# Performance work log

Measured on AMD Instinct MI355X. Metric: run time of the kernel, lower is better.

The kernel has to match this reference:

```python
import jax, jax.numpy as jnp
import numpy as np

B, T, E = 2, 4096, 1024
H = 16
D = E // H  # head_len = 64


def setup_inputs() -> dict:
    key = jax.random.key(0)
    ks = jax.random.split(key, 6)
    s = 1.0 / np.sqrt(E)
    return {
        "x": jax.random.normal(ks[0], (B, T, E), dtype=jnp.float32),
        # torch nn.Linear weights: shape (out, in), y = x @ W.T
        "Wq": jax.random.uniform(ks[1], (E, E), jnp.float32, -s, s),
        "Wk": jax.random.uniform(ks[2], (E, E), jnp.float32, -s, s),
        "Wv": jax.random.uniform(ks[3], (E, E), jnp.float32, -s, s),
        "Wo": jax.random.uniform(ks[4], (E, E), jnp.float32, -s, s),
        "bo": jax.random.uniform(ks[5], (E,), jnp.float32, -s, s),
    }


def reference(x, Wq, Wk, Wv, Wo, bo):
    Bx, Tx, Ex = x.shape
    q = x @ Wq.T
    k = x @ Wk.T
    v = x @ Wv.T
    # (B, T, H, D) -> (B, H, T, D)
    q = q.reshape(Bx, Tx, H, D).transpose(0, 2, 1, 3)
    k = k.reshape(Bx, Tx, H, D).transpose(0, 2, 1, 3)
    v = v.reshape(Bx, Tx, H, D).transpose(0, 2, 1, 3)
    # scores: (B, H, T, T), scaled by sqrt(head_len)
    sim = jnp.einsum("bhqd,bhkd->bhqk", q, k) / jnp.sqrt(jnp.float32(D))
    causal = jnp.tril(jnp.ones((Tx, Tx), dtype=bool))  # True = keep
    sim = jnp.where(causal[None, None], sim, -jnp.inf)
    attn = jax.nn.softmax(sim, axis=-1)
    # dropout_rate = 0.0 (eval) -> identity
    out = jnp.einsum("bhqk,bhkd->bhqd", attn, v)
    out = out.transpose(0, 2, 1, 3).reshape(Bx, Tx, Ex)
    return out @ Wo.T + bo
```

## Files before the change

### kernel.cpp

```cpp
#include <hip/hip_runtime.h>

typedef unsigned short bf16_t;
typedef __bf16 bf16x8 __attribute__((ext_vector_type(8)));
typedef float  v4f   __attribute__((ext_vector_type(4)));
typedef float  v16f  __attribute__((ext_vector_type(16)));
typedef unsigned u32x2 __attribute__((ext_vector_type(2)));

__device__ __forceinline__ bf16_t f2bf(float f) {
    union { float f; unsigned u; } a; a.f = f;
    unsigned r = a.u + 0x7FFFu + ((a.u >> 16) & 1u);
    return (bf16_t)(r >> 16);
}

__device__ __forceinline__ unsigned cvtpk(float lo, float hi) {
    unsigned r;
    asm("v_cvt_pk_bf16_f32 %0, %1, %2" : "=v"(r) : "v"(lo), "v"(hi));
    return r;
}

__device__ __forceinline__ v16f zero16() {
    v16f z;
#pragma unroll
    for (int i = 0; i < 16; ++i) z[i] = 0.f;
    return z;
}

#define GL16(g, l) __builtin_amdgcn_global_load_lds( \
    (__attribute__((address_space(1))) void*)(g),    \
    (__attribute__((address_space(3))) void*)(l), 16, 0, 0)

#define QSCALE 0.18033688011f

__global__ __launch_bounds__(256) void cvt_all(
    const float4* __restrict__ x,  const float4* __restrict__ wq,
    const float4* __restrict__ wk, const float4* __restrict__ wv,
    const float4* __restrict__ wo,
    ushort4* __restrict__ xb, ushort4* __restrict__ wqkv, ushort4* __restrict__ wob) {
    int i = blockIdx.x * 256 + threadIdx.x;
    const float4* s; ushort4* d; int off;
    if (i < 2097152) { s = x; d = xb; off = i; }
    else {
        int wdx = (i - 2097152) >> 18;
        off = (i - 2097152) & 262143;
        if      (wdx == 0) { s = wq; d = wqkv; }
        else if (wdx == 1) { s = wk; d = wqkv + 262144; }
        else if (wdx == 2) { s = wv; d = wqkv + 524288; }
        else               { s = wo; d = wob; }
    }
    float4 v = s[off];
    ushort4 o;
    o.x = f2bf(v.x); o.y = f2bf(v.y); o.z = f2bf(v.z); o.w = f2bf(v.w);
    d[off] = o;
}

__global__ __launch_bounds__(512, 4) void gemm_qkv_kernel(
    const bf16_t* __restrict__ A, const bf16_t* __restrict__ W,
    bf16_t* __restrict__ Qb, bf16_t* __restrict__ Kb, bf16_t* __restrict__ Vtb) {
    __shared__ bf16_t SMEM[16384];
    bf16_t* As = SMEM;
    bf16_t* Bs = SMEM + 8192;
    const int tid = threadIdx.x;
    const int w = tid >> 6, lane = tid & 63;
    const int lrow = lane & 15, lq = lane >> 4;
    const int id_ = blockIdx.y * 24 + blockIdx.x;
    const int xcd_ = id_ & 7, r_ = id_ >> 3;
    const int bys = xcd_ * 4 + (r_ & 3), bxs = r_ >> 2;
    const int m0 = bys * 256, n0 = bxs * 128;
    const int srw = lane >> 2;
    const int sk = (lane & 3) * 8;
    const int wm = (w & 3) * 64, wn = (w >> 2) * 64;
    v4f acc[4][4];
#pragma unroll
    for (int i = 0; i < 4; ++i)
#pragma unroll
        for (int j = 0; j < 4; ++j) acc[i][j] = (v4f){0.f, 0.f, 0.f, 0.f};

    for (int k0 = 0; k0 < 1024; k0 += 32) {
        __syncthreads();
#pragma unroll
        for (int c = 0; c < 3; ++c) {
            int u = w * 3 + c;
            if (u < 16)
                GL16(A + (size_t)(m0 + u * 16 + srw) * 1024 + k0 + sk, (char*)As + u * 1024);
            else
                GL16(W + (size_t)(n0 + (u - 16) * 16 + srw) * 1024 + k0 + sk,
                     (char*)Bs + (u - 16) * 1024);
        }
        __syncthreads();
        bf16x8 af[4], bf[4];
#pragma unroll
        for (int i = 0; i < 4; ++i)
            af[i] = *(const bf16x8*)&As[(wm + i * 16 + lrow) * 32 + lq * 8];
#pragma unroll
        for (int j = 0; j < 4; ++j)
            bf[j] = *(const bf16x8*)&Bs[(wn + j * 16 + lrow) * 32 + lq * 8];
#pragma unroll
        for (int i = 0; i < 4; ++i)
#pragma unroll
            for (int j = 0; j < 4; ++j)
                acc[i][j] = __builtin_amdgcn_mfma_f32_16x16x32_bf16(af[i], bf[j],
                                                                    acc[i][j], 0, 0, 0);
    }

    const int x = bxs;
    const int b = m0 >> 12, t0 = m0 & 4095;
    if (x < 8) {
#pragma unroll
        for (int i = 0; i < 4; ++i)
#pragma unroll
            for (int j = 0; j < 4; ++j)
#pragma unroll
                for (int r = 0; r < 4; ++r) {
                    int t = t0 + wm + i * 16 + lq * 4 + r;
                    int n = n0 + wn + j * 16 + lrow;
                    int h = n >> 6, d = n & 63;
                    Qb[(((size_t)b * 16 + h) * 4096 + t) * 64 + d] =
                        f2bf(acc[i][j][r] * QSCALE);
                }
    } else if (x < 16) {
#pragma unroll
        for (int i = 0; i < 4; ++i)
#pragma unroll
            for (int j = 0; j < 4; ++j)
#pragma unroll
                for (int r = 0; r < 4; ++r) {
                    int t = t0 + wm + i * 16 + lq * 4 + r;
                    int nn = n0 + wn + j * 16 + lrow - 1024;
                    int h = nn >> 6, d = nn & 63;
                    Kb[(((size_t)b * 16 + h) * 4096 + t) * 64 + d] = f2bf(acc[i][j][r]);
                }
    } else {
        const int d0 = n0 - 2048;
#pragma unroll 1
        for (int p = 0; p < 2; ++p) {
            __syncthreads();
            if ((w >> 2) == p) {
#pragma unroll
                for (int i = 0; i < 4; ++i)
#pragma unroll
                    for (int j = 0; j < 4; ++j) {
                        int row = j * 16 + lrow;
                        int swz = (row & 7) << 1;
                        int g = (wm >> 2) + i * 4 + lq;
                        uint2 u;
                        u.x = (unsigned)f2bf(acc[i][j][0]) | ((unsigned)f2bf(acc[i][j][1]) << 16);
                        u.y = (unsigned)f2bf(acc[i][j][2]) | ((unsigned)f2bf(acc[i][j][3]) << 16);
                        *(uint2*)&SMEM[row * 256 + ((g ^ swz) << 2)] = u;
                    }
            }
            __syncthreads();
#pragma unroll
            for (int uu = 0; uu < 4; ++uu) {
                int unit = tid + 512 * uu;
                int row = unit >> 5, seg = unit & 31;
                uint4 val = *(const uint4*)&SMEM[row * 256 + ((seg ^ (row & 7)) << 3)];
                *(uint4*)&Vtb[((size_t)b * 1024 + d0 + p * 64 + row) * 4096 + t0 + seg * 8] = val;
            }
        }
    }
}

#define GEMM_MAINLOOP(A_, W_)                                                          \
    __shared__ bf16_t SMEM[8192];                                                      \
    bf16_t* As = SMEM; bf16_t* Bs = SMEM + 4096;                                       \
    const int tid = threadIdx.x;                                                       \
    const int w = tid >> 6, lane = tid & 63;                                           \
    const int lrow = lane & 15, lq = lane >> 4;                                        \
    const int nwg_ = gridDim.x * gridDim.y;                                            \
    const int id_ = blockIdx.y * gridDim.x + blockIdx.x;                               \
    const int sid_ = (id_ & 7) * (nwg_ >> 3) + (id_ >> 3);                             \
    const int bxs = sid_ % gridDim.x, bys = sid_ / gridDim.x;                          \
    const int m0 = bys * 128, n0 = bxs * 128;                                          \
    const int srow = w * 16 + (lane >> 2);                                             \
    const int sk = (lane & 3) * 8;                                                     \
    const int wm = (w & 1) * 64, wn = (w >> 1) * 64;                                   \
    v4f acc[4][4];                                                                     \
    _Pragma("unroll") for (int i = 0; i < 4; ++i)                                      \
        _Pragma("unroll") for (int j = 0; j < 4; ++j)                                  \
            acc[i][j] = (v4f){0.f, 0.f, 0.f, 0.f};                                     \
    for (int k0 = 0; k0 < 1024; k0 += 32) {                                            \
        __syncthreads();                                                               \
        GL16(A_ + (size_t)(m0 + srow) * 1024 + k0 + sk,      (char*)As + w * 1024);    \
        GL16(A_ + (size_t)(m0 + 64 + srow) * 1024 + k0 + sk, (char*)As + 4096 + w * 1024); \
        GL16(W_ + (size_t)(n0 + srow) * 1024 + k0 + sk,      (char*)Bs + w * 1024);    \
        GL16(W_ + (size_t)(n0 + 64 + srow) * 1024 + k0 + sk, (char*)Bs + 4096 + w * 1024); \
        __syncthreads();                                                               \
        bf16x8 af[4], bf[4];                                                           \
        _Pragma("unroll") for (int i = 0; i < 4; ++i)                                  \
            af[i] = *(const bf16x8*)&As[(wm + i * 16 + lrow) * 32 + lq * 8];           \
        _Pragma("unroll") for (int j = 0; j < 4; ++j)                                  \
            bf[j] = *(const bf16x8*)&Bs[(wn + j * 16 + lrow) * 32 + lq * 8];           \
        _Pragma("unroll") for (int i = 0; i < 4; ++i)                                  \
            _Pragma("unroll") for (int j = 0; j < 4; ++j)                              \
                acc[i][j] = __builtin_amdgcn_mfma_f32_16x16x32_bf16(af[i], bf[j],      \
                                                                    acc[i][j], 0, 0, 0); \
    }

__global__ __launch_bounds__(256) void gemm_out_kernel(
    const bf16_t* __restrict__ A, const bf16_t* __restrict__ W,
    const float* __restrict__ bo, float* __restrict__ out) {
    GEMM_MAINLOOP(A, W)
#pragma unroll
    for (int j = 0; j < 4; ++j) {
        int n = n0 + wn + j * 16 + lrow;
        float bias = bo[n];
#pragma unroll
        for (int i = 0; i < 4; ++i)
#pragma unroll
            for (int r = 0; r < 4; ++r) {
                int m = m0 + wm + i * 16 + lq * 4 + r;
                out[(size_t)m * 1024 + n] = acc[i][j][r] + bias;
            }
    }
}

__global__ __launch_bounds__(256, 2) void attn_kernel(
    const bf16_t* __restrict__ Q, const bf16_t* __restrict__ K,
    const bf16_t* __restrict__ Vt, bf16_t* __restrict__ O) {
    __shared__ bf16_t Kls[2][64 * 64];
    __shared__ bf16_t Vls[2][64 * 64];
    const int tid = threadIdx.x;
    const int w = tid >> 6, lane = tid & 63;
    const int l31 = lane & 31, lh = lane >> 5;

    const int id = blockIdx.y * 16 + blockIdx.x;
    const int g = (id >> 3) & 15;
    const int bh = (id & 7) + ((id >> 7) << 3);

    const bf16_t* Qh = Q + (size_t)bh * (4096 * 64);
    const bf16_t* Kh = K + (size_t)bh * (4096 * 64);
    const bf16_t* Vh = Vt + (size_t)bh * (64 * 4096);
    const int b = bh >> 4, h = bh & 15;

    const int svrow = lane >> 3;
    const int sg8 = ((lane & 7) ^ svrow) * 8;
    const int rx = l31 & 7;

    bf16x8 ones;
#pragma unroll
    for (int i = 0; i < 8; ++i) ones[i] = (__bf16)1.0f;

#pragma unroll 1
    for (int mem = 0; mem < 2; ++mem) {
        const int j = mem ? (31 - g) : g;
        const int q0 = j * 128;
        const int q0w = q0 + w * 32;
        const int nt = 2 * j + 2;
        const int wlast = 2 * j + (w >> 1);
        const int qglob = q0w + l31;

        bf16x8 qf[4];
#pragma unroll
        for (int dk = 0; dk < 4; ++dk)
            qf[dk] = *(const bf16x8*)&Qh[(size_t)(q0w + l31) * 64 + dk * 16 + lh * 8];

        v16f oacc0 = zero16(), oacc1 = zero16(), lacc = zero16();

        auto stage = [&](int kt, int buf) {
            const int kc0 = kt << 6;
#pragma unroll
            for (int i = 0; i < 2; ++i) {
                int r0 = w * 16 + i * 8;
                GL16(Kh + (size_t)(kc0 + r0 + svrow) * 64 + sg8, (char*)&Kls[buf][r0 * 64]);
                GL16(Vh + (size_t)(r0 + svrow) * 4096 + kc0 + sg8, (char*)&Vls[buf][r0 * 64]);
            }
        };

        stage(0, 0);
        for (int kt = 0; kt < nt; ++kt) {
            const int buf = kt & 1;
            __syncthreads();
            if (kt + 1 < nt) stage(kt + 1, buf ^ 1);
            if (kt > wlast) continue;
            const int kc0 = kt << 6;
            const bool diag = (kt == wlast);

            bf16x8 kf[2][4];
#pragma unroll
            for (int th = 0; th < 2; ++th)
#pragma unroll
                for (int dk = 0; dk < 4; ++dk)
                    kf[th][dk] = *(const bf16x8*)
                        &Kls[buf][(th * 32 + l31) * 64 + (((dk * 2 + lh) ^ rx) * 8)];
            bf16x8 vf[2][4];
#pragma unroll
            for (int db = 0; db < 2; ++db)
#pragma unroll
                for (int kb = 0; kb < 4; ++kb)
                    vf[db][kb] = *(const bf16x8*)
                        &Vls[buf][(db * 32 + l31) * 64 + (((kb * 2 + lh) ^ rx) * 8)];

            v16f st0 = zero16(), st1 = zero16();
#pragma unroll
            for (int dk = 0; dk < 4; ++dk) {
                st0 = __builtin_amdgcn_mfma_f32_32x32x16_bf16(kf[0][dk], qf[dk], st0, 0, 0, 0);
                st1 = __builtin_amdgcn_mfma_f32_32x32x16_bf16(kf[1][dk], qf[dk], st1, 0, 0, 0);
            }

            bf16x8 pa[4];
#pragma unroll
            for (int th = 0; th < 2; ++th) {
                float p[16];
#pragma unroll
                for (int rr = 0; rr < 16; ++rr) {
                    float pv = __builtin_amdgcn_exp2f(th ? st1[rr] : st0[rr]);
                    if (diag) {
                        int tg = kc0 + th * 32 + (rr & 3) + 8 * (rr >> 2) + 4 * lh;
                        pv = (tg > qglob) ? 0.f : pv;
                    }
                    p[rr] = pv;
                }
#pragma unroll
                for (int kb2 = 0; kb2 < 2; ++kb2) {
                    unsigned x0 = cvtpk(p[kb2 * 8 + 0], p[kb2 * 8 + 1]);
                    unsigned x1 = cvtpk(p[kb2 * 8 + 2], p[kb2 * 8 + 3]);
                    unsigned y0 = cvtpk(p[kb2 * 8 + 4], p[kb2 * 8 + 5]);
                    unsigned y1 = cvtpk(p[kb2 * 8 + 6], p[kb2 * 8 + 7]);
                    u32x2 ra = __builtin_amdgcn_permlane32_swap(x0, y0, false, false);
                    u32x2 rb = __builtin_amdgcn_permlane32_swap(x1, y1, false, false);
                    union { unsigned u[4]; bf16x8 v; } pu;
                    pu.u[0] = ra.x; pu.u[1] = rb.x;
                    pu.u[2] = ra.y; pu.u[3] = rb.y;
                    pa[th * 2 + kb2] = pu.v;
                }
            }

#pragma unroll
            for (int kb = 0; kb < 4; ++kb) {
                lacc  = __builtin_amdgcn_mfma_f32_32x32x16_bf16(pa[kb], ones,       lacc,  0, 0, 0);
                oacc0 = __builtin_amdgcn_mfma_f32_32x32x16_bf16(pa[kb], vf[0][kb], oacc0, 0, 0, 0);
                oacc1 = __builtin_amdgcn_mfma_f32_32x32x16_bf16(pa[kb], vf[1][kb], oacc1, 0, 0, 0);
            }
        }

#pragma unroll
        for (int rr = 0; rr < 16; ++rr) {
            float rl = 1.0f / lacc[rr];
            int q = q0w + (rr & 3) + 8 * (rr >> 2) + 4 * lh;
            size_t o0 = ((size_t)b * 4096 + q) * 1024 + h * 64;
            O[o0 + l31]      = f2bf(oacc0[rr] * rl);
            O[o0 + 32 + l31] = f2bf(oacc1[rr] * rl);
        }
    }
}

extern "C" void kernel_launch(void* const* d_in, const int* in_sizes, int n_in,
                              void* d_out, int out_size, void* d_ws, size_t ws_size,
                              hipStream_t stream) {
    const float* x  = (const float*)d_in[0];
    const float* Wq = (const float*)d_in[1];
    const float* Wk = (const float*)d_in[2];
    const float* Wv = (const float*)d_in[3];
    const float* Wo = (const float*)d_in[4];
    const float* bo = (const float*)d_in[5];
    float* out = (float*)d_out;

    char* ws = (char*)d_ws;
    bf16_t* xb   = (bf16_t*)(ws + 0);
    bf16_t* Wqkv = (bf16_t*)(ws + 16777216);
    bf16_t* Wob  = (bf16_t*)(ws + 23068672);
    bf16_t* Qb   = (bf16_t*)(ws + 25165824);
    bf16_t* Kb   = (bf16_t*)(ws + 41943040);
    bf16_t* Vtb  = (bf16_t*)(ws + 58720256);
    bf16_t* Ob   = (bf16_t*)(ws + 75497472);

    cvt_all<<<12288, 256, 0, stream>>>((const float4*)x, (const float4*)Wq,
                                       (const float4*)Wk, (const float4*)Wv,
                                       (const float4*)Wo,
                                       (ushort4*)xb, (ushort4*)Wqkv, (ushort4*)Wob);

    gemm_qkv_kernel<<<dim3(24, 32), 512, 0, stream>>>(xb, Wqkv, Qb, Kb, Vtb);

    attn_kernel<<<dim3(16, 32), 256, 0, stream>>>(Qb, Kb, Vtb, Ob);

    gemm_out_kernel<<<dim3(8, 64), 256, 0, stream>>>(Ob, Wob, bo, out);
}
```

Before: 290.9 us.

## Double-buffer LDS tiles in QKV and output GEMM main loops

Both GEMM kernels now keep two LDS buffers and issue the global-to-LDS loads for the next k-slice right after the barrier, before the MFMA work on the current slice. This cuts the loop from two barriers per iteration to one and overlaps memory traffic with matrix math. The cost is more LDS per block: the QKV kernel goes to 48KB, which may lower the number of resident blocks below the launch-bounds target. The old shared GEMM macro is inlined into the output kernel.

Result: no change. 285.7 us (-1.8%).

```diff
diff --git a/kernel.cpp b/kernel.cpp
--- a/kernel.cpp
+++ b/kernel.cpp
@@ -56,9 +56,7 @@
 __global__ __launch_bounds__(512, 4) void gemm_qkv_kernel(
     const bf16_t* __restrict__ A, const bf16_t* __restrict__ W,
     bf16_t* __restrict__ Qb, bf16_t* __restrict__ Kb, bf16_t* __restrict__ Vtb) {
-    __shared__ bf16_t SMEM[16384];
-    bf16_t* As = SMEM;
-    bf16_t* Bs = SMEM + 8192;
+    __shared__ bf16_t SMEM[24576];
     const int tid = threadIdx.x;
     const int w = tid >> 6, lane = tid & 63;
     const int lrow = lane & 15, lq = lane >> 4;
@@ -75,18 +73,27 @@
 #pragma unroll
         for (int j = 0; j < 4; ++j) acc[i][j] = (v4f){0.f, 0.f, 0.f, 0.f};
 
-    for (int k0 = 0; k0 < 1024; k0 += 32) {
-        __syncthreads();
+    auto stage = [&](int k0, int bb) {
+        bf16_t* As_ = SMEM + bb * 12288;
+        bf16_t* Bs_ = As_ + 8192;
 #pragma unroll
         for (int c = 0; c < 3; ++c) {
             int u = w * 3 + c;
             if (u < 16)
-                GL16(A + (size_t)(m0 + u * 16 + srw) * 1024 + k0 + sk, (char*)As + u * 1024);
+                GL16(A + (size_t)(m0 + u * 16 + srw) * 1024 + k0 + sk, (char*)As_ + u * 1024);
             else
                 GL16(W + (size_t)(n0 + (u - 16) * 16 + srw) * 1024 + k0 + sk,
-                     (char*)Bs + (u - 16) * 1024);
+                     (char*)Bs_ + (u - 16) * 1024);
         }
+    };
+
+    stage(0, 0);
+    int buf = 0;
+    for (int ks = 0; ks < 32; ++ks) {
         __syncthreads();
+        if (ks + 1 < 32) stage((ks + 1) * 32, buf ^ 1);
+        const bf16_t* As = SMEM + buf * 12288;
+        const bf16_t* Bs = As + 8192;
         bf16x8 af[4], bf[4];
 #pragma unroll
         for (int i = 0; i < 4; ++i)
@@ -100,6 +107,7 @@
             for (int j = 0; j < 4; ++j)
                 acc[i][j] = __builtin_amdgcn_mfma_f32_16x16x32_bf16(af[i], bf[j],
                                                                     acc[i][j], 0, 0, 0);
+        buf ^= 1;
     }
 
     const int x = bxs;
@@ -160,46 +168,59 @@
     }
 }
 
-#define GEMM_MAINLOOP(A_, W_)                                                          \
-    __shared__ bf16_t SMEM[8192];                                                      \
-    bf16_t* As = SMEM; bf16_t* Bs = SMEM + 4096;                                       \
-    const int tid = threadIdx.x;                                                       \
-    const int w = tid >> 6, lane = tid & 63;                                           \
-    const int lrow = lane & 15, lq = lane >> 4;                                        \
-    const int nwg_ = gridDim.x * gridDim.y;                                            \
-    const int id_ = blockIdx.y * gridDim.x + blockIdx.x;                               \
-    const int sid_ = (id_ & 7) * (nwg_ >> 3) + (id_ >> 3);                             \
-    const int bxs = sid_ % gridDim.x, bys = sid_ / gridDim.x;                          \
-    const int m0 = bys * 128, n0 = bxs * 128;                                          \
-    const int srow = w * 16 + (lane >> 2);                                             \
-    const int sk = (lane & 3) * 8;                                                     \
-    const int wm = (w & 1) * 64, wn = (w >> 1) * 64;                                   \
-    v4f acc[4][4];                                                                     \
-    _Pragma("unroll") for (int i = 0; i < 4; ++i)                                      \
-        _Pragma("unroll") for (int j = 0; j < 4; ++j)                                  \
-            acc[i][j] = (v4f){0.f, 0.f, 0.f, 0.f};                                     \
-    for (int k0 = 0; k0 < 1024; k0 += 32) {                                            \
-        __syncthreads();                                                               \
-        GL16(A_ + (size_t)(m0 + srow) * 1024 + k0 + sk,      (char*)As + w * 1024);    \
-        GL16(A_ + (size_t)(m0 + 64 + srow) * 1024 + k0 + sk, (char*)As + 4096 + w * 1024); \
-        GL16(W_ + (size_t)(n0 + srow) * 1024 + k0 + sk,      (char*)Bs + w * 1024);    \
-        GL16(W_ + (size_t)(n0 + 64 + srow) * 1024 + k0 + sk, (char*)Bs + 4096 + w * 1024); \
-        __syncthreads();                                                               \
-        bf16x8 af[4], bf[4];                                                           \
-        _Pragma("unroll") for (int i = 0; i < 4; ++i)                                  \
-            af[i] = *(const bf16x8*)&As[(wm + i * 16 + lrow) * 32 + lq * 8];           \
-        _Pragma("unroll") for (int j = 0; j < 4; ++j)                                  \
-            bf[j] = *(const bf16x8*)&Bs[(wn + j * 16 + lrow) * 32 + lq * 8];           \
-        _Pragma("unroll") for (int i = 0; i < 4; ++i)                                  \
-            _Pragma("unroll") for (int j = 0; j < 4; ++j)                              \
-                acc[i][j] = __builtin_amdgcn_mfma_f32_16x16x32_bf16(af[i], bf[j],      \
-                                                                    acc[i][j], 0, 0, 0); \
-    }
-
 __global__ __launch_bounds__(256) void gemm_out_kernel(
     const bf16_t* __restrict__ A, const bf16_t* __restrict__ W,
     const float* __restrict__ bo, float* __restrict__ out) {
-    GEMM_MAINLOOP(A, W)
+    __shared__ bf16_t SMEM[16384];
+    const int tid = threadIdx.x;
+    const int w = tid >> 6, lane = tid & 63;
+    const int lrow = lane & 15, lq = lane >> 4;
+    const int nwg_ = gridDim.x * gridDim.y;
+    const int id_ = blockIdx.y * gridDim.x + blockIdx.x;
+    const int sid_ = (id_ & 7) * (nwg_ >> 3) + (id_ >> 3);
+    const int bxs = sid_ % gridDim.x, bys = sid_ / gridDim.x;
+    const int m0 = bys * 128, n0 = bxs * 128;
+    const int srow = w * 16 + (lane >> 2);
+    const int sk = (lane & 3) * 8;
+    const int wm = (w & 1) * 64, wn = (w >> 1) * 64;
+    v4f acc[4][4];
+#pragma unroll
+    for (int i = 0; i < 4; ++i)
+#pragma unroll
+        for (int j = 0; j < 4; ++j) acc[i][j] = (v4f){0.f, 0.f, 0.f, 0.f};
+
+    auto stage = [&](int k0, int bb) {
+        bf16_t* As_ = SMEM + bb * 8192;
+        bf16_t* Bs_ = As_ + 4096;
+        GL16(A + (size_t)(m0 + srow) * 1024 + k0 + sk,      (char*)As_ + w * 1024);
+        GL16(A + (size_t)(m0 + 64 + srow) * 1024 + k0 + sk, (char*)As_ + 4096 + w * 1024);
+        GL16(W + (size_t)(n0 + srow) * 1024 + k0 + sk,      (char*)Bs_ + w * 1024);
+        GL16(W + (size_t)(n0 + 64 + srow) * 1024 + k0 + sk, (char*)Bs_ + 4096 + w * 1024);
+    };
+
+    stage(0, 0);
+    int buf = 0;
+    for (int ks = 0; ks < 32; ++ks) {
+        __syncthreads();
+        if (ks + 1 < 32) stage((ks + 1) * 32, buf ^ 1);
+        const bf16_t* As = SMEM + buf * 8192;
+        const bf16_t* Bs = As + 4096;
+        bf16x8 af[4], bf[4];
+#pragma unroll
+        for (int i = 0; i < 4; ++i)
+            af[i] = *(const bf16x8*)&As[(wm + i * 16 + lrow) * 32 + lq * 8];
+#pragma unroll
+        for (int j = 0; j < 4; ++j)
+            bf[j] = *(const bf16x8*)&Bs[(wn + j * 16 + lrow) * 32 + lq * 8];
+#pragma unroll
+        for (int i = 0; i < 4; ++i)
+#pragma unroll
+            for (int j = 0; j < 4; ++j)
+                acc[i][j] = __builtin_amdgcn_mfma_f32_16x16x32_bf16(af[i], bf[j],
+                                                                    acc[i][j], 0, 0, 0);
+        buf ^= 1;
+    }
+
 #pragma unroll
     for (int j = 0; j < 4; ++j) {
         int n = n0 + wn + j * 16 + lrow;
```
